# Performance work log

Measured on AMD Instinct MI355X. Metric: run time of the kernel, lower is better.

The kernel has to match this reference:

```python
import jax, jax.numpy as jnp
import numpy as np
from jax import lax

N, P, Z, L = 1000, 50000, 10, 5


def setup_inputs() -> dict:
    key = jax.random.key(0)
    ks = jax.random.split(key, 9)
    data = jax.random.normal(ks[0], (N, P), dtype=jnp.float32)
    mean_z = jax.random.normal(ks[1], (N, Z), dtype=jnp.float32)
    A = jax.random.normal(ks[2], (Z, Z), dtype=jnp.float32) * 0.1
    var_z = A @ A.T + 0.01 * jnp.eye(Z, dtype=jnp.float32)  # PSD
    mean_w = jax.random.normal(ks[3], (L, Z, P), dtype=jnp.float32) * 0.01
    var_w = jax.random.uniform(ks[4], (L, Z), dtype=jnp.float32) + 0.1   # positive
    alpha = jax.nn.softmax(jax.random.normal(ks[5], (L, Z, P), dtype=jnp.float32), axis=-1)
    tau_0 = jax.random.uniform(ks[6], (L, Z), dtype=jnp.float32) + 0.5   # positive prior precision
    pi = jax.nn.softmax(jax.random.normal(ks[7], (Z, P), dtype=jnp.float32), axis=-1)
    tau = jnp.array(1.0, dtype=jnp.float32)
    return dict(data=data, mean_z=mean_z, var_z=var_z, mean_w=mean_w,
                var_w=var_w, alpha=alpha, tau_0=tau_0, pi=pi, tau=tau)


def _log_bf(z, s2, s0):
    s0_inv = 1.0 / s0
    s2ps0inv = s2 + s0_inv
    return 0.5 * (jnp.log(s2) - jnp.log(s2ps0inv) + z ** 2 * (s0_inv / s2ps0inv))


def reference(data, mean_z, var_z, mean_w, var_w, alpha, tau_0, pi, tau):
    n_dim = data.shape[0]
    l_dim, z_dim, p_dim = mean_w.shape

    # FactorModel.moments
    mean_zz = mean_z.T @ mean_z + n_dim * var_z            # [z, z]
    # LoadingModel.moments (only mean_w moment is needed)
    W0 = jnp.sum(mean_w * alpha, axis=0)                    # [z, p]

    def factor_body(kdx, carry):
        W, mw, vw, al = carry
        not_k = jnp.where(jnp.arange(z_dim) != kdx, size=z_dim - 1)[0]  # [z-1]
        E_zpzk = mean_zz[kdx][not_k]                        # [z-1]
        E_zzk = mean_zz[kdx, kdx]                           # scalar
        Wk = W[kdx]                                         # [p]
        Wnk = W[not_k]                                      # [z-1, p]
        RtZk = mean_z[:, kdx] @ data - Wnk.T @ E_zpzk       # [p]

        def effect_body(ldx, ecarry):
            Wk, mw, vw, al = ecarry
            Wkl = Wk - mw[ldx, kdx] * al[ldx, kdx]          # [p] residualized
            E_RtZk = RtZk - E_zzk * Wkl                     # [p]
            u_var = jnp.reciprocal(tau * E_zzk + tau_0[ldx, kdx])  # scalar
            u_mean = tau * u_var * E_RtZk                   # [p]
            Z_s = E_RtZk / E_zzk * jnp.sqrt(E_zzk * tau)    # [p]
            s2_s = 1.0 / (E_zzk * tau)
            log_bf = _log_bf(Z_s, s2_s, tau_0[ldx, kdx])
            alpha_kl = jax.nn.softmax(jnp.log(pi[kdx]) + log_bf)   # [p]
            Wk_new = Wkl + u_mean * alpha_kl
            return (Wk_new,
                    mw.at[ldx, kdx].set(u_mean),
                    vw.at[ldx, kdx].set(u_var),
                    al.at[ldx, kdx].set(alpha_kl))

        Wk, mw, vw, al = lax.fori_loop(0, l_dim, effect_body, (Wk, mw, vw, al))
        return (W.at[kdx].set(Wk), mw, vw, al)

    W, mw, vw, al = lax.fori_loop(0, z_dim, factor_body, (W0, mean_w, var_w, alpha))
    return mw, vw, al
```

## Files before the change

kernel.cpp:

```cpp
#include <hip/hip_runtime.h>
#include <math.h>

#define N_DIM 1000
#define P_DIM 50000
#define Z_DIM 10
#define L_DIM 5
#define NSTEP 50

#define NTP 256
#define NBP 196
#define NSPLIT 4
#define NCHUNK 250

#define NT1 256
#define PPT 4
#define PBLK (NT1 * PPT)
#define NBLK 49
#define NWAVES (NBLK * 4)
#define SLOT_STRIDE 256
#define NEG_BIG (-3.0e38f)
#define SPIN_MAX 32768

constexpr size_t ZP       = (size_t)Z_DIM * P_DIM;
constexpr size_t OFF_PART = 0;
constexpr size_t PART_F   = (size_t)NSTEP * SLOT_STRIDE * 2;
constexpr size_t OFF_ZTRP = PART_F;
constexpr size_t OFF_W    = OFF_ZTRP + (size_t)NSPLIT * ZP;
constexpr size_t OFF_ZZ   = OFF_W + ZP;

constexpr size_t OUT_MW = 0;
constexpr size_t OUT_VW = (size_t)L_DIM * Z_DIM * P_DIM;
constexpr size_t OUT_AL = OUT_VW + (size_t)L_DIM * Z_DIM;

__global__ __launch_bounds__(NTP) void precompute_big(const float* __restrict__ data,
                                                      const float* __restrict__ mean_z,
                                                      const float* __restrict__ var_z,
                                                      const float* __restrict__ mw0,
                                                      const float* __restrict__ al0,
                                                      float* __restrict__ ws) {
    if (blockIdx.y == NSPLIT) {
        int bx = blockIdx.x;
        if (bx < Z_DIM * Z_DIM) {
            float* zz = ws + OFF_ZZ;
            int i = bx / Z_DIM, j = bx % Z_DIM;
            float s = 0.f;
            for (int n = threadIdx.x; n < N_DIM; n += NTP)
                s += mean_z[n * Z_DIM + i] * mean_z[n * Z_DIM + j];
            #pragma unroll
            for (int off = 32; off > 0; off >>= 1) s += __shfl_xor(s, off);
            __shared__ float ls[4];
            if ((threadIdx.x & 63) == 0) ls[threadIdx.x >> 6] = s;
            __syncthreads();
            if (threadIdx.x == 0) {
                float t = ls[0] + ls[1] + ls[2] + ls[3];
                zz[bx] = t + (float)N_DIM * var_z[bx];
            }
        } else {
            unsigned long long* part = reinterpret_cast<unsigned long long*>(ws + OFF_PART);
            int idx = (bx - Z_DIM * Z_DIM) * NTP + threadIdx.x;
            if (idx < NSTEP * SLOT_STRIDE) part[idx] = 0ULL;
        }
        return;
    }

    float* ZtRp = ws + OFF_ZTRP + (size_t)blockIdx.y * ZP;
    float* W    = ws + OFF_W;
    __shared__ float mzs[NCHUNK * Z_DIM];
    int n0 = blockIdx.y * NCHUNK;
    for (int i = threadIdx.x; i < NCHUNK * Z_DIM; i += NTP)
        mzs[i] = mean_z[n0 * Z_DIM + i];
    __syncthreads();
    int p = blockIdx.x * NTP + threadIdx.x;
    if (p >= P_DIM) return;

    float acc[Z_DIM];
    #pragma unroll
    for (int z = 0; z < Z_DIM; z++) acc[z] = 0.f;
    for (int r = 0; r < NCHUNK; r++) {
        float d = data[(size_t)(n0 + r) * P_DIM + p];
        #pragma unroll
        for (int z = 0; z < Z_DIM; z++) acc[z] = fmaf(mzs[r * Z_DIM + z], d, acc[z]);
    }
    #pragma unroll
    for (int z = 0; z < Z_DIM; z++) ZtRp[(size_t)z * P_DIM + p] = acc[z];

    if (blockIdx.y == 0) {
        #pragma unroll
        for (int z = 0; z < Z_DIM; z++) {
            float w = 0.f;
            #pragma unroll
            for (int l = 0; l < L_DIM; l++) {
                size_t io = ((size_t)l * Z_DIM + z) * P_DIM + p;
                w = fmaf(mw0[io], al0[io], w);
            }
            W[(size_t)z * P_DIM + p] = w;
        }
    }
}

__global__ __launch_bounds__(NT1) void steps_fused(const float* __restrict__ mw0,
                                                   const float* __restrict__ al0,
                                                   const float* __restrict__ pi,
                                                   const float* __restrict__ tau0,
                                                   const float* __restrict__ taup,
                                                   float* __restrict__ ws,
                                                   float* __restrict__ out) {
    const float* ZtRp = ws + OFF_ZTRP;
    const float* Wg   = ws + OFF_W;
    const float* zz   = ws + OFF_ZZ;
    unsigned long long* part = reinterpret_cast<unsigned long long*>(ws + OFF_PART);
    float* out_mw = out + OUT_MW;
    float* out_vw = out + OUT_VW;
    float* out_al = out + OUT_AL;

    const int tid  = threadIdx.x;
    const int bid  = blockIdx.x;
    const int lane = tid & 63;
    const int wid  = tid >> 6;
    const int gw   = bid * 4 + wid;
    const int p0   = bid * PBLK + tid * PPT;
    const bool valid = p0 < P_DIM;
    const float tau = taup[0];
    const bool need3 = lane < (NWAVES - 192);

    float W[Z_DIM][PPT];
    #pragma unroll
    for (int z = 0; z < Z_DIM; z++)
        #pragma unroll
        for (int i = 0; i < PPT; i++) W[z][i] = 0.f;
    float mw_c[PPT], al_c[PPT], lpi[PPT], zk[PPT];
    #pragma unroll
    for (int i = 0; i < PPT; i++) { mw_c[i] = 0.f; al_c[i] = 0.f; lpi[i] = 0.f; zk[i] = 0.f; }
    if (valid) {
        #pragma unroll
        for (int z = 0; z < Z_DIM; z++) {
            float4 t = *reinterpret_cast<const float4*>(Wg + (size_t)z * P_DIM + p0);
            W[z][0] = t.x; W[z][1] = t.y; W[z][2] = t.z; W[z][3] = t.w;
        }
        float4 tm = *reinterpret_cast<const float4*>(mw0 + p0);
        float4 ta = *reinterpret_cast<const float4*>(al0 + p0);
        mw_c[0] = tm.x; mw_c[1] = tm.y; mw_c[2] = tm.z; mw_c[3] = tm.w;
        al_c[0] = ta.x; al_c[1] = ta.y; al_c[2] = ta.z; al_c[3] = ta.w;
        #pragma unroll
        for (int i = 0; i < PPT; i++) lpi[i] = __logf(pi[p0 + i]);
        #pragma unroll
        for (int y = 0; y < NSPLIT; y++) {
            float4 t = *reinterpret_cast<const float4*>(ZtRp + ((size_t)y * Z_DIM + 0) * P_DIM + p0);
            zk[0] += t.x; zk[1] += t.y; zk[2] += t.z; zk[3] += t.w;
        }
    }

    float wk[PPT], r[PPT];
    #pragma unroll
    for (int i = 0; i < PPT; i++) { wk[i] = 0.f; r[i] = 0.f; }
    int k = 0, l = 0;

    #pragma unroll 1
    for (int s = 0; s < NSTEP; s++) {
        const float Ezz   = zz[k * Z_DIM + k];
        const float t0v   = tau0[l * Z_DIM + k];
        const float u_var = 1.f / (tau * Ezz + t0v);
        const float s2    = 1.f / (Ezz * tau);
        const float s0inv = 1.f / t0v;
        const float cq    = 0.5f * (tau / Ezz) * (s0inv / (s2 + s0inv));

        if (l == 0) {
            #pragma unroll
            for (int i = 0; i < PPT; i++) r[i] = zk[i];
            #pragma unroll
            for (int j = 0; j < Z_DIM; j++) {
                float c = (j == k) ? 0.f : zz[k * Z_DIM + j];
                #pragma unroll
                for (int i = 0; i < PPT; i++) r[i] = fmaf(-c, W[j][i], r[i]);
                if (j == k)
                    #pragma unroll
                    for (int i = 0; i < PPT; i++) wk[i] = W[j][i];
            }
        }

        const size_t io = ((size_t)l * Z_DIM + k) * P_DIM + p0;
        float wkl[PPT], um[PPT], lgt[PPT];
        #pragma unroll
        for (int i = 0; i < PPT; i++) { wkl[i] = 0.f; um[i] = 0.f; lgt[i] = NEG_BIG; }
        if (valid) {
            #pragma unroll
            for (int i = 0; i < PPT; i++) {
                wkl[i] = wk[i] - mw_c[i] * al_c[i];
                float E = fmaf(-Ezz, wkl[i], r[i]);
                um[i]  = tau * u_var * E;
                lgt[i] = fmaf(cq * E, E, lpi[i]);
            }
            float4 sv = make_float4(um[0], um[1], um[2], um[3]);
            *reinterpret_cast<float4*>(out_mw + io) = sv;
        }

        float m4 = fmaxf(fmaxf(lgt[0], lgt[1]), fmaxf(lgt[2], lgt[3]));
        #pragma unroll
        for (int off = 32; off > 0; off >>= 1) m4 = fmaxf(m4, __shfl_xor(m4, off));
        const float Mw = m4;
        float esv[PPT];
        #pragma unroll
        for (int i = 0; i < PPT; i++) esv[i] = __expf(lgt[i] - Mw);
        float s4 = (esv[0] + esv[1]) + (esv[2] + esv[3]);
        #pragma unroll
        for (int off = 32; off > 0; off >>= 1) s4 += __shfl_xor(s4, off);
        if (lane == 0) {
            unsigned long long v = ((unsigned long long)__float_as_uint(s4) << 32)
                                 | (unsigned long long)__float_as_uint(Mw);
            __hip_atomic_store(&part[(size_t)s * SLOT_STRIDE + gw], v, __ATOMIC_RELAXED,
                               __HIP_MEMORY_SCOPE_AGENT);
        }

        int kn = k, ln = l + 1;
        if (ln == L_DIM) { ln = 0; kn++; }
        float mw_n[PPT], al_n[PPT];
        #pragma unroll
        for (int i = 0; i < PPT; i++) { mw_n[i] = 0.f; al_n[i] = 0.f; }
        if (valid && s + 1 < NSTEP) {
            size_t ion = ((size_t)ln * Z_DIM + kn) * P_DIM + p0;
            float4 tm = *reinterpret_cast<const float4*>(mw0 + ion);
            float4 ta = *reinterpret_cast<const float4*>(al0 + ion);
            mw_n[0] = tm.x; mw_n[1] = tm.y; mw_n[2] = tm.z; mw_n[3] = tm.w;
            al_n[0] = ta.x; al_n[1] = ta.y; al_n[2] = ta.z; al_n[3] = ta.w;
            if (ln == 0) {
                #pragma unroll
                for (int i = 0; i < PPT; i++) lpi[i] = __logf(pi[(size_t)kn * P_DIM + p0 + i]);
                #pragma unroll
                for (int i = 0; i < PPT; i++) zk[i] = 0.f;
                #pragma unroll
                for (int y = 0; y < NSPLIT; y++) {
                    float4 t = *reinterpret_cast<const float4*>(
                        ZtRp + ((size_t)y * Z_DIM + kn) * P_DIM + p0);
                    zk[0] += t.x; zk[1] += t.y; zk[2] += t.z; zk[3] += t.w;
                }
            }
        }
        float cc[PPT];
        #pragma unroll
        for (int i = 0; i < PPT; i++) cc[i] = um[i] * esv[i];

        const unsigned long long* sb = part + (size_t)s * SLOT_STRIDE;
        unsigned long long v0 = 0, v1 = 0, v2 = 0;
        unsigned long long v3 = need3 ? 0ULL : (1ULL << 32);
        for (int it = 0; it < SPIN_MAX; it++) {
            if (!(unsigned)(v0 >> 32))
                v0 = __hip_atomic_load(sb + lane,       __ATOMIC_RELAXED, __HIP_MEMORY_SCOPE_AGENT);
            if (!(unsigned)(v1 >> 32))
                v1 = __hip_atomic_load(sb + 64 + lane,  __ATOMIC_RELAXED, __HIP_MEMORY_SCOPE_AGENT);
            if (!(unsigned)(v2 >> 32))
                v2 = __hip_atomic_load(sb + 128 + lane, __ATOMIC_RELAXED, __HIP_MEMORY_SCOPE_AGENT);
            if (!(unsigned)(v3 >> 32))
                v3 = __hip_atomic_load(sb + 192 + lane, __ATOMIC_RELAXED, __HIP_MEMORY_SCOPE_AGENT);
            if ((unsigned)(v0 >> 32) && (unsigned)(v1 >> 32) &&
                (unsigned)(v2 >> 32) && (unsigned)(v3 >> 32)) break;
        }
        float m0 = __uint_as_float((unsigned)v0), e0 = __uint_as_float((unsigned)(v0 >> 32));
        float m1 = __uint_as_float((unsigned)v1), e1 = __uint_as_float((unsigned)(v1 >> 32));
        float m2 = __uint_as_float((unsigned)v2), e2 = __uint_as_float((unsigned)(v2 >> 32));
        float m3 = __uint_as_float((unsigned)v3), e3 = __uint_as_float((unsigned)(v3 >> 32));
        float mm = fmaxf(fmaxf(m0, m1), fmaxf(m2, m3));
        #pragma unroll
        for (int off = 32; off > 0; off >>= 1) mm = fmaxf(mm, __shfl_xor(mm, off));
        const float M = mm;
        float ss = e0 * __expf(m0 - M) + e1 * __expf(m1 - M)
                 + e2 * __expf(m2 - M) + e3 * __expf(m3 - M);
        #pragma unroll
        for (int off = 32; off > 0; off >>= 1) ss += __shfl_xor(ss, off);
        const float scale = __expf(Mw - M) / ss;

        if (valid) {
            float a[PPT];
            #pragma unroll
            for (int i = 0; i < PPT; i++) {
                a[i]  = esv[i] * scale;
                wk[i] = fmaf(cc[i], scale, wkl[i]);
            }
            float4 sv = make_float4(a[0], a[1], a[2], a[3]);
            *reinterpret_cast<float4*>(out_al + io) = sv;
        }
        if (tid == 0 && bid == 0) out_vw[l * Z_DIM + k] = u_var;

        if (l == L_DIM - 1) {
            #pragma unroll
            for (int j = 0; j < Z_DIM; j++)
                if (j == k)
                    #pragma unroll
                    for (int i = 0; i < PPT; i++) W[j][i] = wk[i];
        }
        #pragma unroll
        for (int i = 0; i < PPT; i++) { mw_c[i] = mw_n[i]; al_c[i] = al_n[i]; }
        k = kn; l = ln;
    }
}

extern "C" void kernel_launch(void* const* d_in, const int* in_sizes, int n_in,
                              void* d_out, int out_size, void* d_ws, size_t ws_size,
                              hipStream_t stream) {
    (void)in_sizes; (void)n_in; (void)out_size; (void)ws_size;
    const float* data   = (const float*)d_in[0];
    const float* mean_z = (const float*)d_in[1];
    const float* var_z  = (const float*)d_in[2];
    const float* mw0    = (const float*)d_in[3];
    const float* al0    = (const float*)d_in[5];
    const float* tau0   = (const float*)d_in[6];
    const float* pi     = (const float*)d_in[7];
    const float* taup   = (const float*)d_in[8];
    float* out = (float*)d_out;
    float* ws  = (float*)d_ws;

    precompute_big<<<dim3(NBP, NSPLIT + 1), NTP, 0, stream>>>(data, mean_z, var_z,
                                                              mw0, al0, ws);
    steps_fused<<<NBLK, NT1, 0, stream>>>(mw0, al0, pi, tau0, taup, ws, out);
}
```

Baseline: 481.5 us.

## Double points per thread and poll grid partials from one wave per block

Each thread now handles 8 elements instead of 4, which halves the grid to 25 blocks and 100 waves, so each per-step grid-wide softmax reduction has fewer partials to gather. Only wave 0 of each block spins on the partial slots and combines them, then passes the global max and sum to the other waves through double-buffered shared memory after a __syncthreads. This cuts the polling traffic on the atomic slots, but adds a block barrier every step, doubles register pressure for W and the other per-element arrays, and leaves fewer CUs to carry the streaming loads and stores.

```diff
diff --git a/kernel.cpp b/kernel.cpp
--- a/kernel.cpp
+++ b/kernel.cpp
@@ -13,11 +13,11 @@
 #define NCHUNK 250
 
 #define NT1 256
-#define PPT 4
+#define PPT 8
 #define PBLK (NT1 * PPT)
-#define NBLK 49
+#define NBLK 25
 #define NWAVES (NBLK * 4)
-#define SLOT_STRIDE 256
+#define SLOT_STRIDE 128
 #define NEG_BIG (-3.0e38f)
 #define SPIN_MAX 32768
 
@@ -113,6 +113,8 @@
     float* out_vw = out + OUT_VW;
     float* out_al = out + OUT_AL;
 
+    __shared__ float bro[2][2];
+
     const int tid  = threadIdx.x;
     const int bid  = blockIdx.x;
     const int lane = tid & 63;
@@ -121,7 +123,8 @@
     const int p0   = bid * PBLK + tid * PPT;
     const bool valid = p0 < P_DIM;
     const float tau = taup[0];
-    const bool need3 = lane < (NWAVES - 192);
+    const unsigned long long READY0 =
+        ((unsigned long long)1u << 32) | (unsigned long long)__float_as_uint(NEG_BIG);
 
     float W[Z_DIM][PPT];
     #pragma unroll
@@ -134,19 +137,28 @@
     if (valid) {
         #pragma unroll
         for (int z = 0; z < Z_DIM; z++) {
-            float4 t = *reinterpret_cast<const float4*>(Wg + (size_t)z * P_DIM + p0);
-            W[z][0] = t.x; W[z][1] = t.y; W[z][2] = t.z; W[z][3] = t.w;
-        }
-        float4 tm = *reinterpret_cast<const float4*>(mw0 + p0);
-        float4 ta = *reinterpret_cast<const float4*>(al0 + p0);
-        mw_c[0] = tm.x; mw_c[1] = tm.y; mw_c[2] = tm.z; mw_c[3] = tm.w;
-        al_c[0] = ta.x; al_c[1] = ta.y; al_c[2] = ta.z; al_c[3] = ta.w;
+            float4 a = *reinterpret_cast<const float4*>(Wg + (size_t)z * P_DIM + p0);
+            float4 b = *reinterpret_cast<const float4*>(Wg + (size_t)z * P_DIM + p0 + 4);
+            W[z][0] = a.x; W[z][1] = a.y; W[z][2] = a.z; W[z][3] = a.w;
+            W[z][4] = b.x; W[z][5] = b.y; W[z][6] = b.z; W[z][7] = b.w;
+        }
+        float4 ma = *reinterpret_cast<const float4*>(mw0 + p0);
+        float4 mb = *reinterpret_cast<const float4*>(mw0 + p0 + 4);
+        float4 aa = *reinterpret_cast<const float4*>(al0 + p0);
+        float4 ab = *reinterpret_cast<const float4*>(al0 + p0 + 4);
+        mw_c[0]=ma.x; mw_c[1]=ma.y; mw_c[2]=ma.z; mw_c[3]=ma.w;
+        mw_c[4]=mb.x; mw_c[5]=mb.y; mw_c[6]=mb.z; mw_c[7]=mb.w;
+        al_c[0]=aa.x; al_c[1]=aa.y; al_c[2]=aa.z; al_c[3]=aa.w;
+        al_c[4]=ab.x; al_c[5]=ab.y; al_c[6]=ab.z; al_c[7]=ab.w;
         #pragma unroll
         for (int i = 0; i < PPT; i++) lpi[i] = __logf(pi[p0 + i]);
         #pragma unroll
         for (int y = 0; y < NSPLIT; y++) {
-            float4 t = *reinterpret_cast<const float4*>(ZtRp + ((size_t)y * Z_DIM + 0) * P_DIM + p0);
-            zk[0] += t.x; zk[1] += t.y; zk[2] += t.z; zk[3] += t.w;
+            const float* src = ZtRp + ((size_t)y * Z_DIM + 0) * P_DIM + p0;
+            float4 a = *reinterpret_cast<const float4*>(src);
+            float4 b = *reinterpret_cast<const float4*>(src + 4);
+            zk[0]+=a.x; zk[1]+=a.y; zk[2]+=a.z; zk[3]+=a.w;
+            zk[4]+=b.x; zk[5]+=b.y; zk[6]+=b.z; zk[7]+=b.w;
         }
     }
 
@@ -178,30 +190,29 @@
             }
         }
 
-        const size_t io = ((size_t)l * Z_DIM + k) * P_DIM + p0;
-        float wkl[PPT], um[PPT], lgt[PPT];
-        #pragma unroll
-        for (int i = 0; i < PPT; i++) { wkl[i] = 0.f; um[i] = 0.f; lgt[i] = NEG_BIG; }
+        float wkl[PPT], E[PPT], lgt[PPT];
+        #pragma unroll
+        for (int i = 0; i < PPT; i++) { wkl[i] = 0.f; E[i] = 0.f; lgt[i] = NEG_BIG; }
         if (valid) {
             #pragma unroll
             for (int i = 0; i < PPT; i++) {
                 wkl[i] = wk[i] - mw_c[i] * al_c[i];
-                float E = fmaf(-Ezz, wkl[i], r[i]);
-                um[i]  = tau * u_var * E;
-                lgt[i] = fmaf(cq * E, E, lpi[i]);
-            }
-            float4 sv = make_float4(um[0], um[1], um[2], um[3]);
-            *reinterpret_cast<float4*>(out_mw + io) = sv;
-        }
-
-        float m4 = fmaxf(fmaxf(lgt[0], lgt[1]), fmaxf(lgt[2], lgt[3]));
+                E[i]   = fmaf(-Ezz, wkl[i], r[i]);
+                lgt[i] = fmaf(cq * E[i], E[i], lpi[i]);
+            }
+        }
+        float m4 = lgt[0];
+        #pragma unroll
+        for (int i = 1; i < PPT; i++) m4 = fmaxf(m4, lgt[i]);
         #pragma unroll
         for (int off = 32; off > 0; off >>= 1) m4 = fmaxf(m4, __shfl_xor(m4, off));
         const float Mw = m4;
         float esv[PPT];
         #pragma unroll
         for (int i = 0; i < PPT; i++) esv[i] = __expf(lgt[i] - Mw);
-        float s4 = (esv[0] + esv[1]) + (esv[2] + esv[3]);
+        float s4 = 0.f;
+        #pragma unroll
+        for (int i = 0; i < PPT; i++) s4 += esv[i];
         #pragma unroll
         for (int off = 32; off > 0; off >>= 1) s4 += __shfl_xor(s4, off);
         if (lane == 0) {
@@ -211,6 +222,19 @@
                                __HIP_MEMORY_SCOPE_AGENT);
         }
 
+        const size_t io = ((size_t)l * Z_DIM + k) * P_DIM + p0;
+        float cc[PPT];
+        #pragma unroll
+        for (int i = 0; i < PPT; i++) cc[i] = 0.f;
+        if (valid) {
+            float um[PPT];
+            #pragma unroll
+            for (int i = 0; i < PPT; i++) um[i] = tau * u_var * E[i];
+            *reinterpret_cast<float4*>(out_mw + io)     = make_float4(um[0],um[1],um[2],um[3]);
+            *reinterpret_cast<float4*>(out_mw + io + 4) = make_float4(um[4],um[5],um[6],um[7]);
+            #pragma unroll
+            for (int i = 0; i < PPT; i++) cc[i] = um[i] * esv[i];
+        }
         int kn = k, ln = l + 1;
         if (ln == L_DIM) { ln = 0; kn++; }
         float mw_n[PPT], al_n[PPT];
@@ -218,10 +242,14 @@
         for (int i = 0; i < PPT; i++) { mw_n[i] = 0.f; al_n[i] = 0.f; }
         if (valid && s + 1 < NSTEP) {
             size_t ion = ((size_t)ln * Z_DIM + kn) * P_DIM + p0;
-            float4 tm = *reinterpret_cast<const float4*>(mw0 + ion);
-            float4 ta = *reinterpret_cast<const float4*>(al0 + ion);
-            mw_n[0] = tm.x; mw_n[1] = tm.y; mw_n[2] = tm.z; mw_n[3] = tm.w;
-            al_n[0] = ta.x; al_n[1] = ta.y; al_n[2] = ta.z; al_n[3] = ta.w;
+            float4 ma = *reinterpret_cast<const float4*>(mw0 + ion);
+            float4 mb = *reinterpret_cast<const float4*>(mw0 + ion + 4);
+            float4 aa = *reinterpret_cast<const float4*>(al0 + ion);
+            float4 ab = *reinterpret_cast<const float4*>(al0 + ion + 4);
+            mw_n[0]=ma.x; mw_n[1]=ma.y; mw_n[2]=ma.z; mw_n[3]=ma.w;
+            mw_n[4]=mb.x; mw_n[5]=mb.y; mw_n[6]=mb.z; mw_n[7]=mb.w;
+            al_n[0]=aa.x; al_n[1]=aa.y; al_n[2]=aa.z; al_n[3]=aa.w;
+            al_n[4]=ab.x; al_n[5]=ab.y; al_n[6]=ab.z; al_n[7]=ab.w;
             if (ln == 0) {
                 #pragma unroll
                 for (int i = 0; i < PPT; i++) lpi[i] = __logf(pi[(size_t)kn * P_DIM + p0 + i]);
@@ -229,44 +257,39 @@
                 for (int i = 0; i < PPT; i++) zk[i] = 0.f;
                 #pragma unroll
                 for (int y = 0; y < NSPLIT; y++) {
-                    float4 t = *reinterpret_cast<const float4*>(
-                        ZtRp + ((size_t)y * Z_DIM + kn) * P_DIM + p0);
-                    zk[0] += t.x; zk[1] += t.y; zk[2] += t.z; zk[3] += t.w;
+                    const float* src = ZtRp + ((size_t)y * Z_DIM + kn) * P_DIM + p0;
+                    float4 a = *reinterpret_cast<const float4*>(src);
+                    float4 b = *reinterpret_cast<const float4*>(src + 4);
+                    zk[0]+=a.x; zk[1]+=a.y; zk[2]+=a.z; zk[3]+=a.w;
+                    zk[4]+=b.x; zk[5]+=b.y; zk[6]+=b.z; zk[7]+=b.w;
                 }
             }
         }
-        float cc[PPT];
-        #pragma unroll
-        for (int i = 0; i < PPT; i++) cc[i] = um[i] * esv[i];
-
-        const unsigned long long* sb = part + (size_t)s * SLOT_STRIDE;
-        unsigned long long v0 = 0, v1 = 0, v2 = 0;
-        unsigned long long v3 = need3 ? 0ULL : (1ULL << 32);
-        for (int it = 0; it < SPIN_MAX; it++) {
-            if (!(unsigned)(v0 >> 32))
-                v0 = __hip_atomic_load(sb + lane,       __ATOMIC_RELAXED, __HIP_MEMORY_SCOPE_AGENT);
-            if (!(unsigned)(v1 >> 32))
-                v1 = __hip_atomic_load(sb + 64 + lane,  __ATOMIC_RELAXED, __HIP_MEMORY_SCOPE_AGENT);
-            if (!(unsigned)(v2 >> 32))
-                v2 = __hip_atomic_load(sb + 128 + lane, __ATOMIC_RELAXED, __HIP_MEMORY_SCOPE_AGENT);
-            if (!(unsigned)(v3 >> 32))
-                v3 = __hip_atomic_load(sb + 192 + lane, __ATOMIC_RELAXED, __HIP_MEMORY_SCOPE_AGENT);
-            if ((unsigned)(v0 >> 32) && (unsigned)(v1 >> 32) &&
-                (unsigned)(v2 >> 32) && (unsigned)(v3 >> 32)) break;
-        }
-        float m0 = __uint_as_float((unsigned)v0), e0 = __uint_as_float((unsigned)(v0 >> 32));
-        float m1 = __uint_as_float((unsigned)v1), e1 = __uint_as_float((unsigned)(v1 >> 32));
-        float m2 = __uint_as_float((unsigned)v2), e2 = __uint_as_float((unsigned)(v2 >> 32));
-        float m3 = __uint_as_float((unsigned)v3), e3 = __uint_as_float((unsigned)(v3 >> 32));
-        float mm = fmaxf(fmaxf(m0, m1), fmaxf(m2, m3));
-        #pragma unroll
-        for (int off = 32; off > 0; off >>= 1) mm = fmaxf(mm, __shfl_xor(mm, off));
-        const float M = mm;
-        float ss = e0 * __expf(m0 - M) + e1 * __expf(m1 - M)
-                 + e2 * __expf(m2 - M) + e3 * __expf(m3 - M);
-        #pragma unroll
-        for (int off = 32; off > 0; off >>= 1) ss += __shfl_xor(ss, off);
-        const float scale = __expf(Mw - M) / ss;
+
+        if (wid == 0) {
+            const unsigned long long* sb = part + (size_t)s * SLOT_STRIDE;
+            unsigned long long v0 = 0;
+            unsigned long long v1 = (lane < NWAVES - 64) ? 0ULL : READY0;
+            for (int it = 0; it < SPIN_MAX; it++) {
+                if (!(unsigned)(v0 >> 32))
+                    v0 = __hip_atomic_load(sb + lane,      __ATOMIC_RELAXED, __HIP_MEMORY_SCOPE_AGENT);
+                if (!(unsigned)(v1 >> 32))
+                    v1 = __hip_atomic_load(sb + 64 + lane, __ATOMIC_RELAXED, __HIP_MEMORY_SCOPE_AGENT);
+                if ((unsigned)(v0 >> 32) && (unsigned)(v1 >> 32)) break;
+            }
+            float m0 = __uint_as_float((unsigned)v0), e0 = __uint_as_float((unsigned)(v0 >> 32));
+            float m1 = __uint_as_float((unsigned)v1), e1 = __uint_as_float((unsigned)(v1 >> 32));
+            float mm = fmaxf(m0, m1);
+            #pragma unroll
+            for (int off = 32; off > 0; off >>= 1) mm = fmaxf(mm, __shfl_xor(mm, off));
+            float ss = e0 * __expf(m0 - mm) + e1 * __expf(m1 - mm);
+            #pragma unroll
+            for (int off = 32; off > 0; off >>= 1) ss += __shfl_xor(ss, off);
+            if (lane == 0) { bro[s & 1][0] = mm; bro[s & 1][1] = ss; }
+        }
+        __syncthreads();
+        const float M     = bro[s & 1][0];
+        const float scale = __expf(Mw - M) / bro[s & 1][1];
 
         if (valid) {
             float a[PPT];
@@ -275,8 +298,8 @@
                 a[i]  = esv[i] * scale;
                 wk[i] = fmaf(cc[i], scale, wkl[i]);
             }
-            float4 sv = make_float4(a[0], a[1], a[2], a[3]);
-            *reinterpret_cast<float4*>(out_al + io) = sv;
+            *reinterpret_cast<float4*>(out_al + io)     = make_float4(a[0],a[1],a[2],a[3]);
+            *reinterpret_cast<float4*>(out_al + io + 4) = make_float4(a[4],a[5],a[6],a[7]);
         }
         if (tid == 0 && bid == 0) out_vw[l * Z_DIM + k] = u_var;
 
```

Result: faster. 468.7 us (-2.7%).
